# Optimization experiments

Measured on AMD Instinct MI355X. Metric: run time of the kernel, lower is better.

The kernel has to match this reference:

```python
import jax, jax.numpy as jnp
import numpy as np

B, L, F, H, DIM = 32, 1024, 1024, 1024, 1024


def setup_inputs() -> dict:
    key = jax.random.key(0)
    ks = jax.random.split(key, 8)
    features = jax.random.normal(ks[0], (B, L, F), dtype=jnp.float32)
    hidden = jax.random.normal(ks[1], (B, H), dtype=jnp.float32)
    # Dense layer params (glorot-ish scale)
    W1 = jax.random.normal(ks[2], (F, DIM), dtype=jnp.float32) / np.sqrt(F)
    b1 = jnp.zeros((DIM,), dtype=jnp.float32)
    W2 = jax.random.normal(ks[3], (H, DIM), dtype=jnp.float32) / np.sqrt(H)
    b2 = jnp.zeros((DIM,), dtype=jnp.float32)
    Wp = jax.random.normal(ks[4], (DIM, 1), dtype=jnp.float32) / np.sqrt(DIM)
    bp = jnp.zeros((1,), dtype=jnp.float32)
    return {"features": features, "hidden": hidden, "W1": W1, "b1": b1,
            "W2": W2, "b2": b2, "Wp": Wp, "bp": bp}


def reference(features, hidden, W1, b1, W2, b2, Wp, bp):
    # features: [B, L, F], hidden: [B, H]
    h1 = jnp.einsum('blf,fd->bld', features, W1) + b1          # [B, L, D]
    h2 = (hidden @ W2 + b2)[:, None, :]                         # [B, 1, D]
    att = jnp.tanh(h1 + h2)                                     # [B, L, D]
    score = jnp.einsum('bld,do->blo', att, Wp) + bp             # [B, L, 1]
    attention_weights = jax.nn.softmax(score, axis=1)           # [B, L, 1]
    context_vector = jnp.sum(attention_weights * features, axis=1)  # [B, F]
    return context_vector
```

## Files before the change

### kernel.cpp

```cpp
#include <hip/hip_runtime.h>
#include <hip/hip_bf16.h>


typedef __attribute__((ext_vector_type(8))) __bf16 bf16x8;
typedef __attribute__((ext_vector_type(4))) float f32x4;

#define BM 128
#define BN 128
#define BK 32
#define LDK 40

static __device__ __forceinline__ ushort f2bf(float x) {
  unsigned u = __float_as_uint(x);
  return (ushort)((u + 0x7fffu + ((u >> 16) & 1u)) >> 16);
}

__global__ __launch_bounds__(256) void transpose_w1_kernel(
    const float* __restrict__ W1, ushort* __restrict__ W1T) {
  __shared__ float t[64][65];
  const int tr = blockIdx.y, tc = blockIdx.x, tid = threadIdx.x;
  const int r = tid >> 4;
  const int c4 = (tid & 15) * 4;
#pragma unroll
  for (int p = 0; p < 4; ++p) {
    const int rr = p * 16 + r;
    float4 v = *(const float4*)(W1 + (size_t)(tr * 64 + rr) * 1024 + tc * 64 + c4);
    t[rr][c4] = v.x; t[rr][c4 + 1] = v.y; t[rr][c4 + 2] = v.z; t[rr][c4 + 3] = v.w;
  }
  __syncthreads();
  const int cc = tid >> 3;
  const int r8 = (tid & 7) * 8;
#pragma unroll
  for (int p = 0; p < 2; ++p) {
    const int c = p * 32 + cc;
    ushort tmp[8];
#pragma unroll
    for (int j = 0; j < 8; ++j) tmp[j] = f2bf(t[r8 + j][c]);
    *(int4*)(W1T + (size_t)(tc * 64 + c) * 1024 + tr * 64 + r8) = *(int4*)tmp;
  }
}

__global__ void zero_kernel(float* __restrict__ p) {
  p[(size_t)blockIdx.x * 256 + threadIdx.x] = 0.f;
}

__global__ __launch_bounds__(256) void h2_kernel(
    const float* __restrict__ hidden, const float* __restrict__ W2,
    const float* __restrict__ b2, float* __restrict__ h2) {
  const int d = blockIdx.x * 256 + threadIdx.x;
  const int b = blockIdx.y;
  const int k0 = blockIdx.z * 256;
  __shared__ float h[256];
  h[threadIdx.x] = hidden[b * 1024 + k0 + threadIdx.x];
  __syncthreads();
  float acc = (blockIdx.z == 0) ? b2[d] : 0.f;
#pragma unroll 8
  for (int k = 0; k < 256; ++k)
    acc += h[k] * W2[(size_t)(k0 + k) * 1024 + d];
  atomicAdd(&h2[b * 1024 + d], acc);
}

__global__ __launch_bounds__(256) void gemm_score_kernel(
    const float* __restrict__ feat,
    const ushort* __restrict__ w1t,
    const float* __restrict__ b1,
    const float* __restrict__ h2,
    const float* __restrict__ wp,
    float* __restrict__ score) {
  __shared__ ushort ldsA[BM * LDK];
  __shared__ ushort ldsB[BN * LDK];
  const int tid = threadIdx.x;
  const int row0 = blockIdx.x * BM;
  const int col0 = blockIdx.y * BN;
  const int b = row0 >> 10;

  const int wave = tid >> 6, lane = tid & 63;
  const int wm = wave & 1, wn = wave >> 1;
  const int lrow = lane & 15;
  const int quad = lane >> 4;

  const int arow = tid >> 1;
  const int akof = (tid & 1) * 16;
  const int brow = tid >> 2;
  const int bkof = (tid & 3) * 8;

  f32x4 acc[4][4] = {};

  for (int k0 = 0; k0 < 1024; k0 += BK) {
    {
      const float* ap = feat + (size_t)(row0 + arow) * 1024 + k0 + akof;
      float4 v0 = *(const float4*)(ap + 0);
      float4 v1 = *(const float4*)(ap + 4);
      float4 v2 = *(const float4*)(ap + 8);
      float4 v3 = *(const float4*)(ap + 12);
      __hip_bfloat162 c0 = __float22bfloat162_rn(make_float2(v0.x, v0.y));
      __hip_bfloat162 c1 = __float22bfloat162_rn(make_float2(v0.z, v0.w));
      __hip_bfloat162 c2 = __float22bfloat162_rn(make_float2(v1.x, v1.y));
      __hip_bfloat162 c3 = __float22bfloat162_rn(make_float2(v1.z, v1.w));
      __hip_bfloat162 c4 = __float22bfloat162_rn(make_float2(v2.x, v2.y));
      __hip_bfloat162 c5 = __float22bfloat162_rn(make_float2(v2.z, v2.w));
      __hip_bfloat162 c6 = __float22bfloat162_rn(make_float2(v3.x, v3.y));
      __hip_bfloat162 c7 = __float22bfloat162_rn(make_float2(v3.z, v3.w));
      int4 w0, w1;
      w0.x = *(int*)&c0; w0.y = *(int*)&c1; w0.z = *(int*)&c2; w0.w = *(int*)&c3;
      w1.x = *(int*)&c4; w1.y = *(int*)&c5; w1.z = *(int*)&c6; w1.w = *(int*)&c7;
      *(int4*)&ldsA[arow * LDK + akof] = w0;
      *(int4*)&ldsA[arow * LDK + akof + 8] = w1;
    }
#pragma unroll
    for (int p = 0; p < 2; ++p) {
      const int m = p * 64 + brow;
      *(int4*)&ldsB[m * LDK + bkof] =
          *(const int4*)(w1t + (size_t)(col0 + m) * 1024 + k0 + bkof);
    }
    __syncthreads();
    bf16x8 afrag[4], bfrag[4];
#pragma unroll
    for (int i = 0; i < 4; ++i)
      afrag[i] = *(const bf16x8*)&ldsA[(wm * 64 + i * 16 + lrow) * LDK + quad * 8];
#pragma unroll
    for (int j = 0; j < 4; ++j)
      bfrag[j] = *(const bf16x8*)&ldsB[(wn * 64 + j * 16 + lrow) * LDK + quad * 8];
#pragma unroll
    for (int i = 0; i < 4; ++i)
#pragma unroll
      for (int j = 0; j < 4; ++j)
        acc[i][j] = __builtin_amdgcn_mfma_f32_16x16x32_bf16(
            afrag[i], bfrag[j], acc[i][j], 0, 0, 0);
    __syncthreads();
  }

  float hbv[4], wpv[4];
#pragma unroll
  for (int j = 0; j < 4; ++j) {
    const int d = col0 + wn * 64 + j * 16 + lrow;
    hbv[j] = b1[d] + h2[b * 1024 + d];
    wpv[j] = wp[d];
  }
#pragma unroll
  for (int i = 0; i < 4; ++i) {
#pragma unroll
    for (int r = 0; r < 4; ++r) {
      float s = 0.f;
#pragma unroll
      for (int j = 0; j < 4; ++j)
        s += tanhf(acc[i][j][r] + hbv[j]) * wpv[j];
      s += __shfl_xor(s, 8);
      s += __shfl_xor(s, 4);
      s += __shfl_xor(s, 2);
      s += __shfl_xor(s, 1);
      if (lrow == 0)
        atomicAdd(&score[row0 + wm * 64 + i * 16 + quad * 4 + r], s);
    }
  }
}

__global__ __launch_bounds__(256) void softmax_kernel(
    const float* __restrict__ score, float* __restrict__ w) {
  const int b = blockIdx.x, tid = threadIdx.x;
  const int lane = tid & 63, wv = tid >> 6;
  __shared__ float sm[4], ss[4];
  float v[4];
  float mx = -1e30f;
#pragma unroll
  for (int i = 0; i < 4; ++i) {
    v[i] = score[b * 1024 + i * 256 + tid];
    mx = fmaxf(mx, v[i]);
  }
#pragma unroll
  for (int off = 32; off; off >>= 1) mx = fmaxf(mx, __shfl_xor(mx, off));
  if (lane == 0) sm[wv] = mx;
  __syncthreads();
  mx = fmaxf(fmaxf(sm[0], sm[1]), fmaxf(sm[2], sm[3]));
  float sum = 0.f;
#pragma unroll
  for (int i = 0; i < 4; ++i) {
    v[i] = __expf(v[i] - mx);
    sum += v[i];
  }
#pragma unroll
  for (int off = 32; off; off >>= 1) sum += __shfl_xor(sum, off);
  if (lane == 0) ss[wv] = sum;
  __syncthreads();
  const float inv = 1.f / (ss[0] + ss[1] + ss[2] + ss[3]);
#pragma unroll
  for (int i = 0; i < 4; ++i) w[b * 1024 + i * 256 + tid] = v[i] * inv;
}

__global__ __launch_bounds__(256) void context_kernel(
    const float* __restrict__ w, const float* __restrict__ feat,
    float* __restrict__ out) {
  const int b = blockIdx.y;
  const int l0 = blockIdx.x * 128;
  const int f0 = threadIdx.x * 4;
  __shared__ float wl[128];
  if (threadIdx.x < 128) wl[threadIdx.x] = w[b * 1024 + l0 + threadIdx.x];
  __syncthreads();
  const float* fb = feat + (size_t)b * 1048576 + (size_t)l0 * 1024 + f0;
  float a0 = 0.f, a1 = 0.f, a2 = 0.f, a3 = 0.f;
#pragma unroll 4
  for (int l = 0; l < 128; ++l) {
    float4 v = *(const float4*)(fb + (size_t)l * 1024);
    const float wv = wl[l];
    a0 += wv * v.x;
    a1 += wv * v.y;
    a2 += wv * v.z;
    a3 += wv * v.w;
  }
  float* dst = out + b * 1024 + f0;
  atomicAdd(dst + 0, a0);
  atomicAdd(dst + 1, a1);
  atomicAdd(dst + 2, a2);
  atomicAdd(dst + 3, a3);
}

extern "C" void kernel_launch(void* const* d_in, const int* in_sizes, int n_in,
                              void* d_out, int out_size, void* d_ws, size_t ws_size,
                              hipStream_t stream) {
  const float* feat   = (const float*)d_in[0];
  const float* hidden = (const float*)d_in[1];
  const float* W1     = (const float*)d_in[2];
  const float* b1     = (const float*)d_in[3];
  const float* W2     = (const float*)d_in[4];
  const float* b2     = (const float*)d_in[5];
  const float* Wp     = (const float*)d_in[6];
  float* out = (float*)d_out;

  char* ws = (char*)d_ws;
  ushort* w1t  = (ushort*)ws;
  float* score = (float*)(ws + 2097152);
  float* h2buf = (float*)(ws + 2097152 + 131072);
  float* wts   = (float*)(ws + 2097152 + 262144);

  transpose_w1_kernel<<<dim3(16, 16), 256, 0, stream>>>(W1, w1t);
  zero_kernel<<<256, 256, 0, stream>>>(score);
  zero_kernel<<<128, 256, 0, stream>>>(out);
  h2_kernel<<<dim3(4, 32, 4), 256, 0, stream>>>(hidden, W2, b2, h2buf);
  gemm_score_kernel<<<dim3(256, 8), 256, 0, stream>>>(feat, w1t, b1, h2buf, Wp,
                                                      score);
  softmax_kernel<<<32, 256, 0, stream>>>(score, wts);
  context_kernel<<<dim3(8, 32), 256, 0, stream>>>(wts, feat, out);
}
```

Before: 374.3 us.

## Use direct global-to-LDS loads with swizzle, drop atomics, widen context grid

The GEMM now loads fp32 feature tiles and bf16 W1 tiles straight into LDS with global_load_lds and XOR-swizzled addresses, converting A to bf16 after the LDS read instead of before the store. Score and h2 atomics become per-slice partial buffers that softmax and the GEMM epilogue sum, which removes the score zeroing kernel. The context kernel uses 32-row chunks so it launches four times as many blocks. Staging fp32 A in LDS doubles its LDS footprint and read traffic, and the loop still has no double buffering.

```diff
diff --git a/kernel.cpp b/kernel.cpp
--- a/kernel.cpp
+++ b/kernel.cpp
@@ -8,11 +8,26 @@
 #define BM 128
 #define BN 128
 #define BK 32
-#define LDK 40
 
 static __device__ __forceinline__ ushort f2bf(float x) {
   unsigned u = __float_as_uint(x);
   return (ushort)((u + 0x7fffu + ((u >> 16) & 1u)) >> 16);
+}
+
+typedef __attribute__((address_space(1))) void gbl_t;
+typedef __attribute__((address_space(3))) void lds_t;
+static __device__ __forceinline__ void gl_lds16(const void* g, void* l) {
+  __builtin_amdgcn_global_load_lds((gbl_t*)g, (lds_t*)l, 16, 0, 0);
+}
+
+static __device__ __forceinline__ bf16x8 cvt8(float4 lo, float4 hi) {
+  __hip_bfloat162 c0 = __float22bfloat162_rn({lo.x, lo.y});
+  __hip_bfloat162 c1 = __float22bfloat162_rn({lo.z, lo.w});
+  __hip_bfloat162 c2 = __float22bfloat162_rn({hi.x, hi.y});
+  __hip_bfloat162 c3 = __float22bfloat162_rn({hi.z, hi.w});
+  union { int4 i; bf16x8 v; } u;
+  u.i.x = *(int*)&c0; u.i.y = *(int*)&c1; u.i.z = *(int*)&c2; u.i.w = *(int*)&c3;
+  return u.v;
 }
 
 __global__ __launch_bounds__(256) void transpose_w1_kernel(
@@ -46,29 +61,31 @@
 
 __global__ __launch_bounds__(256) void h2_kernel(
     const float* __restrict__ hidden, const float* __restrict__ W2,
-    const float* __restrict__ b2, float* __restrict__ h2) {
+    const float* __restrict__ b2, float* __restrict__ h2p) {
   const int d = blockIdx.x * 256 + threadIdx.x;
   const int b = blockIdx.y;
-  const int k0 = blockIdx.z * 256;
-  __shared__ float h[256];
-  h[threadIdx.x] = hidden[b * 1024 + k0 + threadIdx.x];
-  __syncthreads();
-  float acc = (blockIdx.z == 0) ? b2[d] : 0.f;
+  const int z = blockIdx.z;
+  const int k0 = z * 128;
+  __shared__ float h[128];
+  if (threadIdx.x < 128) h[threadIdx.x] = hidden[b * 1024 + k0 + threadIdx.x];
+  __syncthreads();
+  float acc = (z == 0) ? b2[d] : 0.f;
 #pragma unroll 8
-  for (int k = 0; k < 256; ++k)
+  for (int k = 0; k < 128; ++k)
     acc += h[k] * W2[(size_t)(k0 + k) * 1024 + d];
-  atomicAdd(&h2[b * 1024 + d], acc);
+  h2p[z * 32768 + b * 1024 + d] = acc;
 }
 
 __global__ __launch_bounds__(256) void gemm_score_kernel(
     const float* __restrict__ feat,
     const ushort* __restrict__ w1t,
     const float* __restrict__ b1,
-    const float* __restrict__ h2,
+    const float* __restrict__ h2p,
     const float* __restrict__ wp,
-    float* __restrict__ score) {
-  __shared__ ushort ldsA[BM * LDK];
-  __shared__ ushort ldsB[BN * LDK];
+    float* __restrict__ score_p) {
+  __shared__ float ldsA[BM * BK];
+  __shared__ ushort ldsB[BN * BK];
+  __shared__ float sred[2][64];
   const int tid = threadIdx.x;
   const int row0 = blockIdx.x * BM;
   const int col0 = blockIdx.y * BN;
@@ -79,54 +96,56 @@
   const int lrow = lane & 15;
   const int quad = lane >> 4;
 
-  const int arow = tid >> 1;
-  const int akof = (tid & 1) * 16;
-  const int brow = tid >> 2;
-  const int bkof = (tid & 3) * 8;
+  int a_go[4], a_ls[4];
+#pragma unroll
+  for (int it = 0; it < 4; ++it) {
+    const int slot = wave * 256 + it * 64 + lane;
+    const int r = slot >> 3, kc = slot & 7;
+    a_go[it] = (row0 + r) * 1024 + (kc ^ (r & 7)) * 4;
+    a_ls[it] = (wave * 256 + it * 64) * 16;
+  }
+  int b_go[2], b_ls[2];
+#pragma unroll
+  for (int it = 0; it < 2; ++it) {
+    const int slot = wave * 128 + it * 64 + lane;
+    const int r = slot >> 2, kc = slot & 3;
+    b_go[it] = (col0 + r) * 1024 + (kc ^ ((r >> 1) & 3)) * 8;
+    b_ls[it] = (wave * 128 + it * 64) * 16;
+  }
 
   f32x4 acc[4][4] = {};
 
   for (int k0 = 0; k0 < 1024; k0 += BK) {
-    {
-      const float* ap = feat + (size_t)(row0 + arow) * 1024 + k0 + akof;
-      float4 v0 = *(const float4*)(ap + 0);
-      float4 v1 = *(const float4*)(ap + 4);
-      float4 v2 = *(const float4*)(ap + 8);
-      float4 v3 = *(const float4*)(ap + 12);
-      __hip_bfloat162 c0 = __float22bfloat162_rn(make_float2(v0.x, v0.y));
-      __hip_bfloat162 c1 = __float22bfloat162_rn(make_float2(v0.z, v0.w));
-      __hip_bfloat162 c2 = __float22bfloat162_rn(make_float2(v1.x, v1.y));
-      __hip_bfloat162 c3 = __float22bfloat162_rn(make_float2(v1.z, v1.w));
-      __hip_bfloat162 c4 = __float22bfloat162_rn(make_float2(v2.x, v2.y));
-      __hip_bfloat162 c5 = __float22bfloat162_rn(make_float2(v2.z, v2.w));
-      __hip_bfloat162 c6 = __float22bfloat162_rn(make_float2(v3.x, v3.y));
-      __hip_bfloat162 c7 = __float22bfloat162_rn(make_float2(v3.z, v3.w));
-      int4 w0, w1;
-      w0.x = *(int*)&c0; w0.y = *(int*)&c1; w0.z = *(int*)&c2; w0.w = *(int*)&c3;
-      w1.x = *(int*)&c4; w1.y = *(int*)&c5; w1.z = *(int*)&c6; w1.w = *(int*)&c7;
-      *(int4*)&ldsA[arow * LDK + akof] = w0;
-      *(int4*)&ldsA[arow * LDK + akof + 8] = w1;
+#pragma unroll
+    for (int it = 0; it < 4; ++it)
+      gl_lds16(feat + a_go[it] + k0, (char*)ldsA + a_ls[it]);
+#pragma unroll
+    for (int it = 0; it < 2; ++it)
+      gl_lds16(w1t + b_go[it] + k0, (char*)ldsB + b_ls[it]);
+    __syncthreads();
+
+    bf16x8 af[4], bfr[4];
+#pragma unroll
+    for (int i = 0; i < 4; ++i) {
+      const int r = wm * 64 + i * 16 + lrow;
+      const int s0 = (quad * 2) ^ (r & 7);
+      const int s1 = (quad * 2 + 1) ^ (r & 7);
+      float4 lo = *(const float4*)&ldsA[r * 32 + s0 * 4];
+      float4 hi = *(const float4*)&ldsA[r * 32 + s1 * 4];
+      af[i] = cvt8(lo, hi);
     }
 #pragma unroll
-    for (int p = 0; p < 2; ++p) {
-      const int m = p * 64 + brow;
-      *(int4*)&ldsB[m * LDK + bkof] =
-          *(const int4*)(w1t + (size_t)(col0 + m) * 1024 + k0 + bkof);
+    for (int j = 0; j < 4; ++j) {
+      const int r = wn * 64 + j * 16 + lrow;
+      const int s = quad ^ ((r >> 1) & 3);
+      bfr[j] = *(const bf16x8*)&ldsB[r * 32 + s * 8];
     }
-    __syncthreads();
-    bf16x8 afrag[4], bfrag[4];
-#pragma unroll
-    for (int i = 0; i < 4; ++i)
-      afrag[i] = *(const bf16x8*)&ldsA[(wm * 64 + i * 16 + lrow) * LDK + quad * 8];
-#pragma unroll
-    for (int j = 0; j < 4; ++j)
-      bfrag[j] = *(const bf16x8*)&ldsB[(wn * 64 + j * 16 + lrow) * LDK + quad * 8];
 #pragma unroll
     for (int i = 0; i < 4; ++i)
 #pragma unroll
       for (int j = 0; j < 4; ++j)
         acc[i][j] = __builtin_amdgcn_mfma_f32_16x16x32_bf16(
-            afrag[i], bfrag[j], acc[i][j], 0, 0, 0);
+            af[i], bfr[j], acc[i][j], 0, 0, 0);
     __syncthreads();
   }
 
@@ -134,9 +153,13 @@
 #pragma unroll
   for (int j = 0; j < 4; ++j) {
     const int d = col0 + wn * 64 + j * 16 + lrow;
-    hbv[j] = b1[d] + h2[b * 1024 + d];
+    float hv = b1[d];
+#pragma unroll
+    for (int p = 0; p < 8; ++p) hv += h2p[p * 32768 + b * 1024 + d];
+    hbv[j] = hv;
     wpv[j] = wp[d];
   }
+  float rsum[4][4];
 #pragma unroll
   for (int i = 0; i < 4; ++i) {
 #pragma unroll
@@ -149,14 +172,31 @@
       s += __shfl_xor(s, 4);
       s += __shfl_xor(s, 2);
       s += __shfl_xor(s, 1);
-      if (lrow == 0)
-        atomicAdd(&score[row0 + wm * 64 + i * 16 + quad * 4 + r], s);
+      rsum[i][r] = s;
     }
   }
+  if (wn == 1 && lrow == 0) {
+#pragma unroll
+    for (int i = 0; i < 4; ++i)
+#pragma unroll
+      for (int r = 0; r < 4; ++r)
+        sred[wm][i * 16 + quad * 4 + r] = rsum[i][r];
+  }
+  __syncthreads();
+  if (wn == 0 && lrow == 0) {
+#pragma unroll
+    for (int i = 0; i < 4; ++i)
+#pragma unroll
+      for (int r = 0; r < 4; ++r) {
+        const int ro = wm * 64 + i * 16 + quad * 4 + r;
+        score_p[(size_t)blockIdx.y * 32768 + row0 + ro] =
+            rsum[i][r] + sred[wm][ro & 63];
+      }
+  }
 }
 
 __global__ __launch_bounds__(256) void softmax_kernel(
-    const float* __restrict__ score, float* __restrict__ w) {
+    const float* __restrict__ score_p, float* __restrict__ w) {
   const int b = blockIdx.x, tid = threadIdx.x;
   const int lane = tid & 63, wv = tid >> 6;
   __shared__ float sm[4], ss[4];
@@ -164,8 +204,12 @@
   float mx = -1e30f;
 #pragma unroll
   for (int i = 0; i < 4; ++i) {
-    v[i] = score[b * 1024 + i * 256 + tid];
-    mx = fmaxf(mx, v[i]);
+    const int idx = b * 1024 + i * 256 + tid;
+    float s = 0.f;
+#pragma unroll
+    for (int p = 0; p < 8; ++p) s += score_p[p * 32768 + idx];
+    v[i] = s;
+    mx = fmaxf(mx, s);
   }
 #pragma unroll
   for (int off = 32; off; off >>= 1) mx = fmaxf(mx, __shfl_xor(mx, off));
@@ -191,15 +235,15 @@
     const float* __restrict__ w, const float* __restrict__ feat,
     float* __restrict__ out) {
   const int b = blockIdx.y;
-  const int l0 = blockIdx.x * 128;
+  const int l0 = blockIdx.x * 32;
   const int f0 = threadIdx.x * 4;
-  __shared__ float wl[128];
-  if (threadIdx.x < 128) wl[threadIdx.x] = w[b * 1024 + l0 + threadIdx.x];
+  __shared__ float wl[32];
+  if (threadIdx.x < 32) wl[threadIdx.x] = w[b * 1024 + l0 + threadIdx.x];
   __syncthreads();
   const float* fb = feat + (size_t)b * 1048576 + (size_t)l0 * 1024 + f0;
   float a0 = 0.f, a1 = 0.f, a2 = 0.f, a3 = 0.f;
-#pragma unroll 4
-  for (int l = 0; l < 128; ++l) {
+#pragma unroll 8
+  for (int l = 0; l < 32; ++l) {
     float4 v = *(const float4*)(fb + (size_t)l * 1024);
     const float wv = wl[l];
     a0 += wv * v.x;
@@ -227,17 +271,16 @@
   float* out = (float*)d_out;
 
   char* ws = (char*)d_ws;
-  ushort* w1t  = (ushort*)ws;
-  float* score = (float*)(ws + 2097152);
-  float* h2buf = (float*)(ws + 2097152 + 131072);
-  float* wts   = (float*)(ws + 2097152 + 262144);
+  ushort* w1t    = (ushort*)ws;
+  float* score_p = (float*)(ws + 2097152);
+  float* h2p     = (float*)(ws + 3145728);
+  float* wts     = (float*)(ws + 4194304);
 
   transpose_w1_kernel<<<dim3(16, 16), 256, 0, stream>>>(W1, w1t);
-  zero_kernel<<<256, 256, 0, stream>>>(score);
+  h2_kernel<<<dim3(4, 32, 8), 256, 0, stream>>>(hidden, W2, b2, h2p);
+  gemm_score_kernel<<<dim3(256, 8), 256, 0, stream>>>(feat, w1t, b1, h2p, Wp,
+                                                      score_p);
+  softmax_kernel<<<32, 256, 0, stream>>>(score_p, wts);
   zero_kernel<<<128, 256, 0, stream>>>(out);
-  h2_kernel<<<dim3(4, 32, 4), 256, 0, stream>>>(hidden, W2, b2, h2buf);
-  gemm_score_kernel<<<dim3(256, 8), 256, 0, stream>>>(feat, w1t, b1, h2buf, Wp,
-                                                      score);
-  softmax_kernel<<<32, 256, 0, stream>>>(score, wts);
-  context_kernel<<<dim3(8, 32), 256, 0, stream>>>(wts, feat, out);
-}
+  context_kernel<<<dim3(32, 32), 256, 0, stream>>>(wts, feat, out);
+}
```

After: 392.2 us. 4.8% more time.
